# Kernel tuning notes

Hardware: AMD Instinct MI355X
Metric: run time of the kernel (lower is better)

## Reference

```python
import jax, jax.numpy as jnp
import numpy as np

B, N, F, L = 8, 2048, 128, 2
SLOPE = 0.1  # LeakyReLU negative slope

def lrelu(v):
    return jnp.where(v >= 0, v, SLOPE * v)

def setup_inputs() -> dict:
    key = jax.random.key(0)
    ks = jax.random.split(key, 7)
    scale = 1.0 / np.sqrt(F)
    return {
        "x": jax.random.normal(ks[0], (B, N, F), dtype=jnp.float32),
        "W3": jax.random.normal(ks[1], (L, F, F), dtype=jnp.float32) * scale,
        "b3": jnp.zeros((L, F), dtype=jnp.float32),
        "W4": jax.random.normal(ks[2], (L, F, F), dtype=jnp.float32) * scale,
        "b4": jnp.zeros((L, F), dtype=jnp.float32),
        "W5": jax.random.normal(ks[3], (L, F, F), dtype=jnp.float32) * scale,
        "b5": jnp.zeros((L, F), dtype=jnp.float32),
    }

def reference(x, W3, b3, W4, b4, W5, b5):
    # GraphStack of L GraphLayer modules, mes_type '0':
    #   weight_ij = dot(LeakyReLU(g3(n_i)), LeakyReLU(g4(n_j)))
    #   message_i = mean_{j != i} weight_ij * n_j
    #   n_i_out   = LeakyReLU(g5(message_i)) + n_i
    n = x.shape[1]
    for l in range(W3.shape[0]):
        w1 = lrelu(jnp.einsum('bnf,fg->bng', x, W3[l]) + b3[l])  # [B,N,F]
        w2 = lrelu(jnp.einsum('bnf,fg->bng', x, W4[l]) + b4[l])  # [B,N,F]
        wt = jnp.einsum('bif,bjf->bij', w1, w2)                  # pairwise weights [B,N,N]
        diag = jnp.einsum('bif,bif->bi', w1, w2)                 # self weights to exclude
        msg = (jnp.einsum('bij,bjf->bif', wt, x) - diag[..., None] * x) / (n - 1)
        x = lrelu(jnp.einsum('bif,fg->big', msg, W5[l]) + b5[l]) + x
    return x
```

## Files before the change

### kernel.cpp

```cpp
#include <hip/hip_runtime.h>

#define BB 8
#define NN 2048
#define FF 128
#define NL 2
#define SLOPE 0.1f
#define NROW (BB * NN)
#define XS_STRIDE 136

typedef __attribute__((ext_vector_type(8))) short short8;
typedef __attribute__((ext_vector_type(4))) float f32x4;

__device__ __forceinline__ float lrelu(float v) { return v >= 0.f ? v : SLOPE * v; }

__device__ __forceinline__ ushort f2bf(float f) {
    uint u = __float_as_uint(f);
    return (ushort)((u + 0x7fffu + ((u >> 16) & 1u)) >> 16);
}

__global__ __launch_bounds__(256) void k_prep(
    const float* __restrict__ W3, const float* __restrict__ W4,
    const float* __restrict__ W5, ushort* __restrict__ Wt)
{
    const int idx = blockIdx.x * 256 + threadIdx.x;
    const int m = idx >> 14;
    const int rem = idx & 16383;
    const int f = rem & 127;
    const int g = rem >> 7;
    const int l = m / 3, w = m % 3;
    const float* src = (w == 0) ? W3 : (w == 1) ? W4 : W5;
    Wt[m * 16384 + g * 128 + f] = f2bf(src[l * 16384 + f * 128 + g]);
}

__global__ __launch_bounds__(512) void k_w12(
    const float* __restrict__ x, const ushort* __restrict__ w3t,
    const ushort* __restrict__ w4t, const float* __restrict__ b3,
    const float* __restrict__ b4, ushort* __restrict__ w1b,
    ushort* __restrict__ w2t, ushort* __restrict__ xt,
    float* __restrict__ diag)
{
    __shared__ ushort xs[64 * XS_STRIDE];
    __shared__ float diag_s[64];

    const int tid = threadIdx.x;
    const int row0 = blockIdx.x * 64;
    const int b = row0 >> 11;
    const int jloc0 = row0 & 2047;

    if (tid < 64) diag_s[tid] = 0.f;

    const float4* xg4 = (const float4*)(x + (size_t)row0 * FF);
#pragma unroll
    for (int i = 0; i < 4; i++) {
        const int f4 = i * 512 + tid;
        const int row = f4 >> 5;
        const int k = (f4 & 31) * 4;
        float4 v = xg4[f4];
        ushort4 h;
        h.x = f2bf(v.x); h.y = f2bf(v.y); h.z = f2bf(v.z); h.w = f2bf(v.w);
        *(ushort4*)&xs[row * XS_STRIDE + k] = h;
    }
    __syncthreads();

    {
        const int g = tid >> 2;
        const int h = tid & 3;
        uint p[8];
#pragma unroll
        for (int jj = 0; jj < 8; jj++) {
            const uint lo = xs[(h * 16 + jj * 2) * XS_STRIDE + g];
            const uint hi = xs[(h * 16 + jj * 2 + 1) * XS_STRIDE + g];
            p[jj] = lo | (hi << 16);
        }
        uint4* dst = (uint4*)&xt[(size_t)b * (FF * NN) + (size_t)g * NN + jloc0 + h * 16];
        dst[0] = make_uint4(p[0], p[1], p[2], p[3]);
        dst[1] = make_uint4(p[4], p[5], p[6], p[7]);
    }

    const int lane = tid & 63;
    const int wave = tid >> 6;
    const int c = lane & 15;
    const int quad = lane >> 4;
    const int n = wave * 16 + c;

    f32x4 acc1[4], acc2[4];
#pragma unroll
    for (int rt = 0; rt < 4; rt++) { acc1[rt] = (f32x4)0.f; acc2[rt] = (f32x4)0.f; }

#pragma unroll
    for (int kk = 0; kk < 4; kk++) {
        short8 bf3 = *(const short8*)&w3t[n * 128 + kk * 32 + quad * 8];
        short8 bf4 = *(const short8*)&w4t[n * 128 + kk * 32 + quad * 8];
#pragma unroll
        for (int rt = 0; rt < 4; rt++) {
            short8 a = *(const short8*)&xs[(rt * 16 + c) * XS_STRIDE + kk * 32 + quad * 8];
            acc1[rt] = __builtin_amdgcn_mfma_f32_16x16x32_bf16(a, bf3, acc1[rt], 0, 0, 0);
            acc2[rt] = __builtin_amdgcn_mfma_f32_16x16x32_bf16(a, bf4, acc2[rt], 0, 0, 0);
        }
    }

    const int gcol = wave * 16 + c;
    const float bb3 = b3[gcol], bb4 = b4[gcol];
    float dpar[4][4];

#pragma unroll
    for (int rt = 0; rt < 4; rt++) {
        ushort w2p[4];
#pragma unroll
        for (int r = 0; r < 4; r++) {
            const float v1 = lrelu(acc1[rt][r] + bb3);
            const float v2 = lrelu(acc2[rt][r] + bb4);
            const int grow = row0 + rt * 16 + quad * 4 + r;
            w1b[(size_t)grow * FF + gcol] = f2bf(v1);
            w2p[r] = f2bf(v2);
            dpar[rt][r] = v1 * v2;
        }
        const uint lo = (uint)w2p[0] | ((uint)w2p[1] << 16);
        const uint hi = (uint)w2p[2] | ((uint)w2p[3] << 16);
        uint2* dst = (uint2*)&w2t[(size_t)b * (FF * NN) + (size_t)gcol * NN +
                                  jloc0 + rt * 16 + quad * 4];
        *dst = make_uint2(lo, hi);
    }

#pragma unroll
    for (int rt = 0; rt < 4; rt++) {
#pragma unroll
        for (int r = 0; r < 4; r++) {
            float dp = dpar[rt][r];
            dp += __shfl_xor(dp, 1, 64);
            dp += __shfl_xor(dp, 2, 64);
            dp += __shfl_xor(dp, 4, 64);
            dp += __shfl_xor(dp, 8, 64);
            if (c == 0) atomicAdd(&diag_s[rt * 16 + quad * 4 + r], dp);
        }
    }
    __syncthreads();
    if (tid < 64) diag[row0 + tid] = diag_s[tid];
}

__global__ __launch_bounds__(256) void k_S2(
    const ushort* __restrict__ xt, const ushort* __restrict__ w2t,
    ushort* __restrict__ St)
{
    __shared__ float red[4][512];
    const int tid = threadIdx.x;
    const int lane = tid & 63;
    const int wave = tid >> 6;
    const int c = lane & 15;
    const int quad = lane >> 4;

    const int b  = blockIdx.x >> 5;
    const int gq = (blockIdx.x >> 3) & 3;
    const int fs = blockIdx.x & 7;

    const ushort* xtb = xt + (size_t)b * (FF * NN);
    const ushort* w2b = w2t + (size_t)b * (FF * NN);

    const int j0 = wave * 512 + quad * 8;
    const ushort* a0p = &xtb[(gq * 32 + c) * NN + j0];
    const ushort* a1p = &xtb[(gq * 32 + 16 + c) * NN + j0];
    const ushort* bp  = &w2b[(fs * 16 + c) * NN + j0];

    f32x4 acc0 = (f32x4)0.f, acc1 = (f32x4)0.f;
#pragma unroll
    for (int it = 0; it < 16; it++) {
        short8 a0 = *(const short8*)(a0p + it * 32);
        short8 a1 = *(const short8*)(a1p + it * 32);
        short8 bf = *(const short8*)(bp + it * 32);
        acc0 = __builtin_amdgcn_mfma_f32_16x16x32_bf16(a0, bf, acc0, 0, 0, 0);
        acc1 = __builtin_amdgcn_mfma_f32_16x16x32_bf16(a1, bf, acc1, 0, 0, 0);
    }

#pragma unroll
    for (int r = 0; r < 4; r++) {
        red[wave][(quad * 4 + r) * 16 + c] = acc0[r];
        red[wave][(16 + quad * 4 + r) * 16 + c] = acc1[r];
    }
    __syncthreads();

#pragma unroll
    for (int i = 0; i < 2; i++) {
        const int idx = i * 256 + tid;
        const float s = red[0][idx] + red[1][idx] + red[2][idx] + red[3][idx];
        const int gl = idx >> 4;
        const int fl = idx & 15;
        St[(size_t)b * (FF * FF) + (size_t)(gq * 32 + gl) * FF + fs * 16 + fl] = f2bf(s);
    }
}

__global__ __launch_bounds__(512) void k_out(
    const float* __restrict__ x, const ushort* __restrict__ w1b,
    const ushort* __restrict__ St, const float* __restrict__ diag,
    const ushort* __restrict__ w5t, const float* __restrict__ b5,
    float* __restrict__ out)
{
    __shared__ ushort w1s[64 * XS_STRIDE];
    __shared__ ushort ms[64 * XS_STRIDE];

    const int tid = threadIdx.x;
    const int row0 = blockIdx.x * 64;
    const int b = row0 >> 11;
    const ushort* Sb = St + (size_t)b * (FF * FF);

#pragma unroll
    for (int i = 0; i < 2; i++) {
        const int off = (i * 512 + tid) * 8;
        const int row = off >> 7;
        const int k = off & 127;
        short8 v = *(const short8*)&w1b[(size_t)row0 * FF + off];
        *(short8*)&w1s[row * XS_STRIDE + k] = v;
    }
    __syncthreads();

    const int lane = tid & 63;
    const int wave = tid >> 6;
    const int c = lane & 15;
    const int quad = lane >> 4;
    const int n = wave * 16 + c;

    f32x4 accm[4];
#pragma unroll
    for (int rt = 0; rt < 4; rt++) accm[rt] = (f32x4)0.f;

#pragma unroll
    for (int kk = 0; kk < 4; kk++) {
        short8 bf = *(const short8*)&Sb[n * 128 + kk * 32 + quad * 8];
#pragma unroll
        for (int rt = 0; rt < 4; rt++) {
            short8 a = *(const short8*)&w1s[(rt * 16 + c) * XS_STRIDE + kk * 32 + quad * 8];
            accm[rt] = __builtin_amdgcn_mfma_f32_16x16x32_bf16(a, bf, accm[rt], 0, 0, 0);
        }
    }

    const float inv = 1.f / (float)(NN - 1);
    const int gcol = wave * 16 + c;
    float xsv[4][4];
#pragma unroll
    for (int rt = 0; rt < 4; rt++) {
        float dg[4];
#pragma unroll
        for (int r = 0; r < 4; r++) dg[r] = diag[row0 + rt * 16 + quad * 4 + r];
#pragma unroll
        for (int r = 0; r < 4; r++) {
            const int lrow = rt * 16 + quad * 4 + r;
            const float xv = x[(size_t)(row0 + lrow) * FF + gcol];
            xsv[rt][r] = xv;
            const float m = (accm[rt][r] - dg[r] * xv) * inv;
            ms[lrow * XS_STRIDE + gcol] = f2bf(m);
        }
    }
    __syncthreads();

    f32x4 acc2[4];
#pragma unroll
    for (int rt = 0; rt < 4; rt++) acc2[rt] = (f32x4)0.f;

#pragma unroll
    for (int kk = 0; kk < 4; kk++) {
        short8 bf = *(const short8*)&w5t[n * 128 + kk * 32 + quad * 8];
#pragma unroll
        for (int rt = 0; rt < 4; rt++) {
            short8 a = *(const short8*)&ms[(rt * 16 + c) * XS_STRIDE + kk * 32 + quad * 8];
            acc2[rt] = __builtin_amdgcn_mfma_f32_16x16x32_bf16(a, bf, acc2[rt], 0, 0, 0);
        }
    }

    const float bb = b5[gcol];
#pragma unroll
    for (int rt = 0; rt < 4; rt++) {
#pragma unroll
        for (int r = 0; r < 4; r++) {
            const int grow = row0 + rt * 16 + quad * 4 + r;
            out[(size_t)grow * FF + gcol] = lrelu(acc2[rt][r] + bb) + xsv[rt][r];
        }
    }
}

__global__ __launch_bounds__(512) void k_out_w12(
    const float* __restrict__ x, const ushort* __restrict__ w1b_in,
    const ushort* __restrict__ St, const float* __restrict__ diag_in,
    const ushort* __restrict__ w5t, const float* __restrict__ b5,
    float* __restrict__ out,
    const ushort* __restrict__ w3t, const ushort* __restrict__ w4t,
    const float* __restrict__ b3, const float* __restrict__ b4,
    ushort* __restrict__ w1b, ushort* __restrict__ w2t,
    ushort* __restrict__ xt, float* __restrict__ diag)
{
    __shared__ ushort sA[64 * XS_STRIDE];
    __shared__ ushort sB[64 * XS_STRIDE];
    __shared__ float diag_s[64];

    const int tid = threadIdx.x;
    const int row0 = blockIdx.x * 64;
    const int b = row0 >> 11;
    const int jloc0 = row0 & 2047;
    const ushort* Sb = St + (size_t)b * (FF * FF);

    if (tid < 64) diag_s[tid] = 0.f;

#pragma unroll
    for (int i = 0; i < 2; i++) {
        const int off = (i * 512 + tid) * 8;
        const int row = off >> 7;
        const int k = off & 127;
        short8 v = *(const short8*)&w1b_in[(size_t)row0 * FF + off];
        *(short8*)&sA[row * XS_STRIDE + k] = v;
    }
    __syncthreads();

    const int lane = tid & 63;
    const int wave = tid >> 6;
    const int c = lane & 15;
    const int quad = lane >> 4;
    const int n = wave * 16 + c;
    const int gcol = wave * 16 + c;

    f32x4 accm[4];
#pragma unroll
    for (int rt = 0; rt < 4; rt++) accm[rt] = (f32x4)0.f;

#pragma unroll
    for (int kk = 0; kk < 4; kk++) {
        short8 bf = *(const short8*)&Sb[n * 128 + kk * 32 + quad * 8];
#pragma unroll
        for (int rt = 0; rt < 4; rt++) {
            short8 a = *(const short8*)&sA[(rt * 16 + c) * XS_STRIDE + kk * 32 + quad * 8];
            accm[rt] = __builtin_amdgcn_mfma_f32_16x16x32_bf16(a, bf, accm[rt], 0, 0, 0);
        }
    }

    const float inv = 1.f / (float)(NN - 1);
    float xsv[4][4];
#pragma unroll
    for (int rt = 0; rt < 4; rt++) {
        float dg[4];
#pragma unroll
        for (int r = 0; r < 4; r++) dg[r] = diag_in[row0 + rt * 16 + quad * 4 + r];
#pragma unroll
        for (int r = 0; r < 4; r++) {
            const int lrow = rt * 16 + quad * 4 + r;
            const float xv = x[(size_t)(row0 + lrow) * FF + gcol];
            xsv[rt][r] = xv;
            const float m = (accm[rt][r] - dg[r] * xv) * inv;
            sB[lrow * XS_STRIDE + gcol] = f2bf(m);
        }
    }
    __syncthreads();

    f32x4 acc2[4];
#pragma unroll
    for (int rt = 0; rt < 4; rt++) acc2[rt] = (f32x4)0.f;

#pragma unroll
    for (int kk = 0; kk < 4; kk++) {
        short8 bf = *(const short8*)&w5t[n * 128 + kk * 32 + quad * 8];
#pragma unroll
        for (int rt = 0; rt < 4; rt++) {
            short8 a = *(const short8*)&sB[(rt * 16 + c) * XS_STRIDE + kk * 32 + quad * 8];
            acc2[rt] = __builtin_amdgcn_mfma_f32_16x16x32_bf16(a, bf, acc2[rt], 0, 0, 0);
        }
    }

    const float bb = b5[gcol];
#pragma unroll
    for (int rt = 0; rt < 4; rt++) {
#pragma unroll
        for (int r = 0; r < 4; r++) {
            const int lrow = rt * 16 + quad * 4 + r;
            const float ov = lrelu(acc2[rt][r] + bb) + xsv[rt][r];
            out[(size_t)(row0 + lrow) * FF + gcol] = ov;
            sA[lrow * XS_STRIDE + gcol] = f2bf(ov);
        }
    }
    __syncthreads();

    {
        const int g = tid >> 2;
        const int h = tid & 3;
        uint p[8];
#pragma unroll
        for (int jj = 0; jj < 8; jj++) {
            const uint lo = sA[(h * 16 + jj * 2) * XS_STRIDE + g];
            const uint hi = sA[(h * 16 + jj * 2 + 1) * XS_STRIDE + g];
            p[jj] = lo | (hi << 16);
        }
        uint4* dst = (uint4*)&xt[(size_t)b * (FF * NN) + (size_t)g * NN + jloc0 + h * 16];
        dst[0] = make_uint4(p[0], p[1], p[2], p[3]);
        dst[1] = make_uint4(p[4], p[5], p[6], p[7]);
    }

    f32x4 acc1n[4], acc2n[4];
#pragma unroll
    for (int rt = 0; rt < 4; rt++) { acc1n[rt] = (f32x4)0.f; acc2n[rt] = (f32x4)0.f; }

#pragma unroll
    for (int kk = 0; kk < 4; kk++) {
        short8 bf3 = *(const short8*)&w3t[n * 128 + kk * 32 + quad * 8];
        short8 bf4 = *(const short8*)&w4t[n * 128 + kk * 32 + quad * 8];
#pragma unroll
        for (int rt = 0; rt < 4; rt++) {
            short8 a = *(const short8*)&sA[(rt * 16 + c) * XS_STRIDE + kk * 32 + quad * 8];
            acc1n[rt] = __builtin_amdgcn_mfma_f32_16x16x32_bf16(a, bf3, acc1n[rt], 0, 0, 0);
            acc2n[rt] = __builtin_amdgcn_mfma_f32_16x16x32_bf16(a, bf4, acc2n[rt], 0, 0, 0);
        }
    }

    const float bb3 = b3[gcol], bb4 = b4[gcol];
    float dpar[4][4];
#pragma unroll
    for (int rt = 0; rt < 4; rt++) {
        ushort w2p[4];
#pragma unroll
        for (int r = 0; r < 4; r++) {
            const float v1 = lrelu(acc1n[rt][r] + bb3);
            const float v2 = lrelu(acc2n[rt][r] + bb4);
            const int grow = row0 + rt * 16 + quad * 4 + r;
            w1b[(size_t)grow * FF + gcol] = f2bf(v1);
            w2p[r] = f2bf(v2);
            dpar[rt][r] = v1 * v2;
        }
        const uint lo = (uint)w2p[0] | ((uint)w2p[1] << 16);
        const uint hi = (uint)w2p[2] | ((uint)w2p[3] << 16);
        uint2* dst = (uint2*)&w2t[(size_t)b * (FF * NN) + (size_t)gcol * NN +
                                  jloc0 + rt * 16 + quad * 4];
        *dst = make_uint2(lo, hi);
    }

#pragma unroll
    for (int rt = 0; rt < 4; rt++) {
#pragma unroll
        for (int r = 0; r < 4; r++) {
            float dp = dpar[rt][r];
            dp += __shfl_xor(dp, 1, 64);
            dp += __shfl_xor(dp, 2, 64);
            dp += __shfl_xor(dp, 4, 64);
            dp += __shfl_xor(dp, 8, 64);
            if (c == 0) atomicAdd(&diag_s[rt * 16 + quad * 4 + r], dp);
        }
    }
    __syncthreads();
    if (tid < 64) diag[row0 + tid] = diag_s[tid];
}

extern "C" void kernel_launch(void* const* d_in, const int* in_sizes, int n_in,
                              void* d_out, int out_size, void* d_ws, size_t ws_size,
                              hipStream_t stream)
{
    const float* x  = (const float*)d_in[0];
    const float* W3 = (const float*)d_in[1];
    const float* b3 = (const float*)d_in[2];
    const float* W4 = (const float*)d_in[3];
    const float* b4 = (const float*)d_in[4];
    const float* W5 = (const float*)d_in[5];
    const float* b5 = (const float*)d_in[6];
    float* out = (float*)d_out;

    char* ws = (char*)d_ws;
    ushort* w1b   = (ushort*)(ws);
    ushort* w2t   = (ushort*)(ws + ((size_t)4  << 20));
    ushort* xt    = (ushort*)(ws + ((size_t)8  << 20));
    float*  diag  = (float*) (ws + ((size_t)12 << 20));
    ushort* St    = (ushort*)(ws + ((size_t)13 << 20));
    ushort* Wt    = (ushort*)(ws + ((size_t)14 << 20));

    const ushort* w3t0 = Wt;
    const ushort* w4t0 = Wt + 16384;
    const ushort* w5t0 = Wt + 2 * 16384;
    const ushort* w3t1 = Wt + 3 * 16384;
    const ushort* w4t1 = Wt + 4 * 16384;
    const ushort* w5t1 = Wt + 5 * 16384;

    const int rowBlocks = NROW / 64;

    k_prep<<<384, 256, 0, stream>>>(W3, W4, W5, Wt);

    k_w12<<<rowBlocks, 512, 0, stream>>>(x, w3t0, w4t0, b3, b4, w1b, w2t, xt, diag);
    k_S2<<<256, 256, 0, stream>>>(xt, w2t, St);
    k_out_w12<<<rowBlocks, 512, 0, stream>>>(x, w1b, St, diag, w5t0, b5, out,
                                             w3t1, w4t1, b3 + FF, b4 + FF,
                                             w1b, w2t, xt, diag);
    k_S2<<<256, 256, 0, stream>>>(xt, w2t, St);
    k_out<<<rowBlocks, 512, 0, stream>>>(out, w1b, St, diag, w5t1, b5 + FF, out);
}
```

Measured before the change: 120.6 us.

## Fuse all stages into one cooperative persistent kernel with grid syncs

```diff
diff --git a/kernel.cpp b/kernel.cpp
--- a/kernel.cpp
+++ b/kernel.cpp
@@ -1,9 +1,11 @@
 #include <hip/hip_runtime.h>
+#include <hip/hip_cooperative_groups.h>
+
+namespace cg = cooperative_groups;
 
 #define BB 8
 #define NN 2048
 #define FF 128
-#define NL 2
 #define SLOPE 0.1f
 #define NROW (BB * NN)
 #define XS_STRIDE 136
@@ -18,428 +20,408 @@
     return (ushort)((u + 0x7fffu + ((u >> 16) & 1u)) >> 16);
 }
 
-__global__ __launch_bounds__(256) void k_prep(
-    const float* __restrict__ W3, const float* __restrict__ W4,
-    const float* __restrict__ W5, ushort* __restrict__ Wt)
+__device__ __forceinline__ void s2_phase(
+    const ushort* __restrict__ xt, const ushort* __restrict__ w2t,
+    ushort* __restrict__ St, float* red,
+    int bid, int tid, int wave, int c, int quad)
 {
-    const int idx = blockIdx.x * 256 + threadIdx.x;
-    const int m = idx >> 14;
-    const int rem = idx & 16383;
-    const int f = rem & 127;
-    const int g = rem >> 7;
-    const int l = m / 3, w = m % 3;
-    const float* src = (w == 0) ? W3 : (w == 1) ? W4 : W5;
-    Wt[m * 16384 + g * 128 + f] = f2bf(src[l * 16384 + f * 128 + g]);
+    const int b  = bid >> 5;
+    const int gq = (bid >> 3) & 3;
+    const int fs = bid & 7;
+
+    const ushort* xtb = xt + (size_t)b * (FF * NN);
+    const ushort* w2b = w2t + (size_t)b * (FF * NN);
+
+    const int j0 = wave * 256 + quad * 8;
+    const ushort* a0p = &xtb[(gq * 32 + c) * NN + j0];
+    const ushort* a1p = &xtb[(gq * 32 + 16 + c) * NN + j0];
+    const ushort* bp  = &w2b[(fs * 16 + c) * NN + j0];
+
+    f32x4 acc0 = (f32x4)0.f, acc1 = (f32x4)0.f;
+#pragma unroll
+    for (int it = 0; it < 8; it++) {
+        short8 a0 = *(const short8*)(a0p + it * 32);
+        short8 a1 = *(const short8*)(a1p + it * 32);
+        short8 bf = *(const short8*)(bp + it * 32);
+        acc0 = __builtin_amdgcn_mfma_f32_16x16x32_bf16(a0, bf, acc0, 0, 0, 0);
+        acc1 = __builtin_amdgcn_mfma_f32_16x16x32_bf16(a1, bf, acc1, 0, 0, 0);
+    }
+
+#pragma unroll
+    for (int r = 0; r < 4; r++) {
+        red[wave * 512 + (quad * 4 + r) * 16 + c] = acc0[r];
+        red[wave * 512 + (16 + quad * 4 + r) * 16 + c] = acc1[r];
+    }
+    __syncthreads();
+
+    {
+        float s = 0.f;
+#pragma unroll
+        for (int w = 0; w < 8; w++) s += red[w * 512 + tid];
+        const int gl = tid >> 4;
+        const int fl = tid & 15;
+        St[(size_t)b * (FF * FF) + (size_t)(gq * 32 + gl) * FF + fs * 16 + fl] = f2bf(s);
+    }
+    __syncthreads();
 }
 
-__global__ __launch_bounds__(512) void k_w12(
-    const float* __restrict__ x, const ushort* __restrict__ w3t,
-    const ushort* __restrict__ w4t, const float* __restrict__ b3,
-    const float* __restrict__ b4, ushort* __restrict__ w1b,
-    ushort* __restrict__ w2t, ushort* __restrict__ xt,
-    float* __restrict__ diag)
+__global__ __launch_bounds__(512) void k_all(
+    const float* __restrict__ x,
+    const float* __restrict__ W3, const float* __restrict__ b3,
+    const float* __restrict__ W4, const float* __restrict__ b4,
+    const float* __restrict__ W5, const float* __restrict__ b5,
+    float* __restrict__ out,
+    ushort* __restrict__ w1b, ushort* __restrict__ w2t,
+    ushort* __restrict__ xt, float* __restrict__ diag,
+    ushort* __restrict__ St, ushort* __restrict__ Wt)
 {
-    __shared__ ushort xs[64 * XS_STRIDE];
+    __shared__ ushort smem[2 * 64 * XS_STRIDE];
     __shared__ float diag_s[64];
 
+    cg::grid_group grid = cg::this_grid();
+
     const int tid = threadIdx.x;
-    const int row0 = blockIdx.x * 64;
-    const int b = row0 >> 11;
-    const int jloc0 = row0 & 2047;
-
-    if (tid < 64) diag_s[tid] = 0.f;
-
-    const float4* xg4 = (const float4*)(x + (size_t)row0 * FF);
-#pragma unroll
-    for (int i = 0; i < 4; i++) {
-        const int f4 = i * 512 + tid;
-        const int row = f4 >> 5;
-        const int k = (f4 & 31) * 4;
-        float4 v = xg4[f4];
-        ushort4 h;
-        h.x = f2bf(v.x); h.y = f2bf(v.y); h.z = f2bf(v.z); h.w = f2bf(v.w);
-        *(ushort4*)&xs[row * XS_STRIDE + k] = h;
-    }
-    __syncthreads();
-
-    {
-        const int g = tid >> 2;
-        const int h = tid & 3;
-        uint p[8];
-#pragma unroll
-        for (int jj = 0; jj < 8; jj++) {
-            const uint lo = xs[(h * 16 + jj * 2) * XS_STRIDE + g];
-            const uint hi = xs[(h * 16 + jj * 2 + 1) * XS_STRIDE + g];
-            p[jj] = lo | (hi << 16);
-        }
-        uint4* dst = (uint4*)&xt[(size_t)b * (FF * NN) + (size_t)g * NN + jloc0 + h * 16];
-        dst[0] = make_uint4(p[0], p[1], p[2], p[3]);
-        dst[1] = make_uint4(p[4], p[5], p[6], p[7]);
-    }
-
+    const int bid = blockIdx.x;
     const int lane = tid & 63;
     const int wave = tid >> 6;
     const int c = lane & 15;
     const int quad = lane >> 4;
     const int n = wave * 16 + c;
-
-    f32x4 acc1[4], acc2[4];
-#pragma unroll
-    for (int rt = 0; rt < 4; rt++) { acc1[rt] = (f32x4)0.f; acc2[rt] = (f32x4)0.f; }
-
-#pragma unroll
-    for (int kk = 0; kk < 4; kk++) {
-        short8 bf3 = *(const short8*)&w3t[n * 128 + kk * 32 + quad * 8];
-        short8 bf4 = *(const short8*)&w4t[n * 128 + kk * 32 + quad * 8];
-#pragma unroll
-        for (int rt = 0; rt < 4; rt++) {
-            short8 a = *(const short8*)&xs[(rt * 16 + c) * XS_STRIDE + kk * 32 + quad * 8];
-            acc1[rt] = __builtin_amdgcn_mfma_f32_16x16x32_bf16(a, bf3, acc1[rt], 0, 0, 0);
-            acc2[rt] = __builtin_amdgcn_mfma_f32_16x16x32_bf16(a, bf4, acc2[rt], 0, 0, 0);
-        }
-    }
-
-    const int gcol = wave * 16 + c;
-    const float bb3 = b3[gcol], bb4 = b4[gcol];
-    float dpar[4][4];
-
-#pragma unroll
-    for (int rt = 0; rt < 4; rt++) {
-        ushort w2p[4];
-#pragma unroll
-        for (int r = 0; r < 4; r++) {
-            const float v1 = lrelu(acc1[rt][r] + bb3);
-            const float v2 = lrelu(acc2[rt][r] + bb4);
-            const int grow = row0 + rt * 16 + quad * 4 + r;
-            w1b[(size_t)grow * FF + gcol] = f2bf(v1);
-            w2p[r] = f2bf(v2);
-            dpar[rt][r] = v1 * v2;
-        }
-        const uint lo = (uint)w2p[0] | ((uint)w2p[1] << 16);
-        const uint hi = (uint)w2p[2] | ((uint)w2p[3] << 16);
-        uint2* dst = (uint2*)&w2t[(size_t)b * (FF * NN) + (size_t)gcol * NN +
-                                  jloc0 + rt * 16 + quad * 4];
-        *dst = make_uint2(lo, hi);
-    }
-
-#pragma unroll
-    for (int rt = 0; rt < 4; rt++) {
-#pragma unroll
-        for (int r = 0; r < 4; r++) {
-            float dp = dpar[rt][r];
-            dp += __shfl_xor(dp, 1, 64);
-            dp += __shfl_xor(dp, 2, 64);
-            dp += __shfl_xor(dp, 4, 64);
-            dp += __shfl_xor(dp, 8, 64);
-            if (c == 0) atomicAdd(&diag_s[rt * 16 + quad * 4 + r], dp);
-        }
-    }
-    __syncthreads();
-    if (tid < 64) diag[row0 + tid] = diag_s[tid];
-}
-
-__global__ __launch_bounds__(256) void k_S2(
-    const ushort* __restrict__ xt, const ushort* __restrict__ w2t,
-    ushort* __restrict__ St)
-{
-    __shared__ float red[4][512];
-    const int tid = threadIdx.x;
-    const int lane = tid & 63;
-    const int wave = tid >> 6;
-    const int c = lane & 15;
-    const int quad = lane >> 4;
-
-    const int b  = blockIdx.x >> 5;
-    const int gq = (blockIdx.x >> 3) & 3;
-    const int fs = blockIdx.x & 7;
-
-    const ushort* xtb = xt + (size_t)b * (FF * NN);
-    const ushort* w2b = w2t + (size_t)b * (FF * NN);
-
-    const int j0 = wave * 512 + quad * 8;
-    const ushort* a0p = &xtb[(gq * 32 + c) * NN + j0];
-    const ushort* a1p = &xtb[(gq * 32 + 16 + c) * NN + j0];
-    const ushort* bp  = &w2b[(fs * 16 + c) * NN + j0];
-
-    f32x4 acc0 = (f32x4)0.f, acc1 = (f32x4)0.f;
-#pragma unroll
-    for (int it = 0; it < 16; it++) {
-        short8 a0 = *(const short8*)(a0p + it * 32);
-        short8 a1 = *(const short8*)(a1p + it * 32);
-        short8 bf = *(const short8*)(bp + it * 32);
-        acc0 = __builtin_amdgcn_mfma_f32_16x16x32_bf16(a0, bf, acc0, 0, 0, 0);
-        acc1 = __builtin_amdgcn_mfma_f32_16x16x32_bf16(a1, bf, acc1, 0, 0, 0);
-    }
-
-#pragma unroll
-    for (int r = 0; r < 4; r++) {
-        red[wave][(quad * 4 + r) * 16 + c] = acc0[r];
-        red[wave][(16 + quad * 4 + r) * 16 + c] = acc1[r];
-    }
-    __syncthreads();
-
-#pragma unroll
-    for (int i = 0; i < 2; i++) {
-        const int idx = i * 256 + tid;
-        const float s = red[0][idx] + red[1][idx] + red[2][idx] + red[3][idx];
-        const int gl = idx >> 4;
-        const int fl = idx & 15;
-        St[(size_t)b * (FF * FF) + (size_t)(gq * 32 + gl) * FF + fs * 16 + fl] = f2bf(s);
-    }
-}
-
-__global__ __launch_bounds__(512) void k_out(
-    const float* __restrict__ x, const ushort* __restrict__ w1b,
-    const ushort* __restrict__ St, const float* __restrict__ diag,
-    const ushort* __restrict__ w5t, const float* __restrict__ b5,
-    float* __restrict__ out)
-{
-    __shared__ ushort w1s[64 * XS_STRIDE];
-    __shared__ ushort ms[64 * XS_STRIDE];
-
-    const int tid = threadIdx.x;
-    const int row0 = blockIdx.x * 64;
-    const int b = row0 >> 11;
-    const ushort* Sb = St + (size_t)b * (FF * FF);
-
-#pragma unroll
-    for (int i = 0; i < 2; i++) {
-        const int off = (i * 512 + tid) * 8;
-        const int row = off >> 7;
-        const int k = off & 127;
-        short8 v = *(const short8*)&w1b[(size_t)row0 * FF + off];
-        *(short8*)&w1s[row * XS_STRIDE + k] = v;
-    }
-    __syncthreads();
-
-    const int lane = tid & 63;
-    const int wave = tid >> 6;
-    const int c = lane & 15;
-    const int quad = lane >> 4;
-    const int n = wave * 16 + c;
-
-    f32x4 accm[4];
-#pragma unroll
-    for (int rt = 0; rt < 4; rt++) accm[rt] = (f32x4)0.f;
-
-#pragma unroll
-    for (int kk = 0; kk < 4; kk++) {
-        short8 bf = *(const short8*)&Sb[n * 128 + kk * 32 + quad * 8];
-#pragma unroll
-        for (int rt = 0; rt < 4; rt++) {
-            short8 a = *(const short8*)&w1s[(rt * 16 + c) * XS_STRIDE + kk * 32 + quad * 8];
-            accm[rt] = __builtin_amdgcn_mfma_f32_16x16x32_bf16(a, bf, accm[rt], 0, 0, 0);
-        }
-    }
-
-    const float inv = 1.f / (float)(NN - 1);
-    const int gcol = wave * 16 + c;
-    float xsv[4][4];
-#pragma unroll
-    for (int rt = 0; rt < 4; rt++) {
-        float dg[4];
-#pragma unroll
-        for (int r = 0; r < 4; r++) dg[r] = diag[row0 + rt * 16 + quad * 4 + r];
-#pragma unroll
-        for (int r = 0; r < 4; r++) {
-            const int lrow = rt * 16 + quad * 4 + r;
-            const float xv = x[(size_t)(row0 + lrow) * FF + gcol];
-            xsv[rt][r] = xv;
-            const float m = (accm[rt][r] - dg[r] * xv) * inv;
-            ms[lrow * XS_STRIDE + gcol] = f2bf(m);
-        }
-    }
-    __syncthreads();
-
-    f32x4 acc2[4];
-#pragma unroll
-    for (int rt = 0; rt < 4; rt++) acc2[rt] = (f32x4)0.f;
-
-#pragma unroll
-    for (int kk = 0; kk < 4; kk++) {
-        short8 bf = *(const short8*)&w5t[n * 128 + kk * 32 + quad * 8];
-#pragma unroll
-        for (int rt = 0; rt < 4; rt++) {
-            short8 a = *(const short8*)&ms[(rt * 16 + c) * XS_STRIDE + kk * 32 + quad * 8];
-            acc2[rt] = __builtin_amdgcn_mfma_f32_16x16x32_bf16(a, bf, acc2[rt], 0, 0, 0);
-        }
-    }
-
-    const float bb = b5[gcol];
-#pragma unroll
-    for (int rt = 0; rt < 4; rt++) {
-#pragma unroll
-        for (int r = 0; r < 4; r++) {
-            const int grow = row0 + rt * 16 + quad * 4 + r;
-            out[(size_t)grow * FF + gcol] = lrelu(acc2[rt][r] + bb) + xsv[rt][r];
-        }
-    }
-}
-
-__global__ __launch_bounds__(512) void k_out_w12(
-    const float* __restrict__ x, const ushort* __restrict__ w1b_in,
-    const ushort* __restrict__ St, const float* __restrict__ diag_in,
-    const ushort* __restrict__ w5t, const float* __restrict__ b5,
-    float* __restrict__ out,
-    const ushort* __restrict__ w3t, const ushort* __restrict__ w4t,
-    const float* __restrict__ b3, const float* __restrict__ b4,
-    ushort* __restrict__ w1b, ushort* __restrict__ w2t,
-    ushort* __restrict__ xt, float* __restrict__ diag)
-{
-    __shared__ ushort sA[64 * XS_STRIDE];
-    __shared__ ushort sB[64 * XS_STRIDE];
-    __shared__ float diag_s[64];
-
-    const int tid = threadIdx.x;
-    const int row0 = blockIdx.x * 64;
+    const int gcol = n;
+
+    const ushort* w3t0 = Wt;
+    const ushort* w4t0 = Wt + 16384;
+    const ushort* w5t0 = Wt + 2 * 16384;
+    const ushort* w3t1 = Wt + 3 * 16384;
+    const ushort* w4t1 = Wt + 4 * 16384;
+    const ushort* w5t1 = Wt + 5 * 16384;
+
+    const int row0 = bid * 64;
     const int b = row0 >> 11;
     const int jloc0 = row0 & 2047;
-    const ushort* Sb = St + (size_t)b * (FF * FF);
-
-    if (tid < 64) diag_s[tid] = 0.f;
-
-#pragma unroll
-    for (int i = 0; i < 2; i++) {
-        const int off = (i * 512 + tid) * 8;
-        const int row = off >> 7;
-        const int k = off & 127;
-        short8 v = *(const short8*)&w1b_in[(size_t)row0 * FF + off];
-        *(short8*)&sA[row * XS_STRIDE + k] = v;
-    }
-    __syncthreads();
-
-    const int lane = tid & 63;
-    const int wave = tid >> 6;
-    const int c = lane & 15;
-    const int quad = lane >> 4;
-    const int n = wave * 16 + c;
-    const int gcol = wave * 16 + c;
-
-    f32x4 accm[4];
-#pragma unroll
-    for (int rt = 0; rt < 4; rt++) accm[rt] = (f32x4)0.f;
-
-#pragma unroll
-    for (int kk = 0; kk < 4; kk++) {
-        short8 bf = *(const short8*)&Sb[n * 128 + kk * 32 + quad * 8];
-#pragma unroll
-        for (int rt = 0; rt < 4; rt++) {
-            short8 a = *(const short8*)&sA[(rt * 16 + c) * XS_STRIDE + kk * 32 + quad * 8];
-            accm[rt] = __builtin_amdgcn_mfma_f32_16x16x32_bf16(a, bf, accm[rt], 0, 0, 0);
-        }
-    }
-
     const float inv = 1.f / (float)(NN - 1);
-    float xsv[4][4];
-#pragma unroll
-    for (int rt = 0; rt < 4; rt++) {
-        float dg[4];
-#pragma unroll
-        for (int r = 0; r < 4; r++) dg[r] = diag_in[row0 + rt * 16 + quad * 4 + r];
-#pragma unroll
-        for (int r = 0; r < 4; r++) {
-            const int lrow = rt * 16 + quad * 4 + r;
-            const float xv = x[(size_t)(row0 + lrow) * FF + gcol];
-            xsv[rt][r] = xv;
-            const float m = (accm[rt][r] - dg[r] * xv) * inv;
-            sB[lrow * XS_STRIDE + gcol] = f2bf(m);
-        }
-    }
-    __syncthreads();
-
-    f32x4 acc2[4];
-#pragma unroll
-    for (int rt = 0; rt < 4; rt++) acc2[rt] = (f32x4)0.f;
-
-#pragma unroll
-    for (int kk = 0; kk < 4; kk++) {
-        short8 bf = *(const short8*)&w5t[n * 128 + kk * 32 + quad * 8];
-#pragma unroll
-        for (int rt = 0; rt < 4; rt++) {
-            short8 a = *(const short8*)&sB[(rt * 16 + c) * XS_STRIDE + kk * 32 + quad * 8];
-            acc2[rt] = __builtin_amdgcn_mfma_f32_16x16x32_bf16(a, bf, acc2[rt], 0, 0, 0);
-        }
-    }
-
-    const float bb = b5[gcol];
-#pragma unroll
-    for (int rt = 0; rt < 4; rt++) {
-#pragma unroll
-        for (int r = 0; r < 4; r++) {
-            const int lrow = rt * 16 + quad * 4 + r;
-            const float ov = lrelu(acc2[rt][r] + bb) + xsv[rt][r];
-            out[(size_t)(row0 + lrow) * FF + gcol] = ov;
-            sA[lrow * XS_STRIDE + gcol] = f2bf(ov);
-        }
-    }
-    __syncthreads();
 
     {
-        const int g = tid >> 2;
-        const int h = tid & 3;
-        uint p[8];
-#pragma unroll
-        for (int jj = 0; jj < 8; jj++) {
-            const uint lo = sA[(h * 16 + jj * 2) * XS_STRIDE + g];
-            const uint hi = sA[(h * 16 + jj * 2 + 1) * XS_STRIDE + g];
-            p[jj] = lo | (hi << 16);
-        }
-        uint4* dst = (uint4*)&xt[(size_t)b * (FF * NN) + (size_t)g * NN + jloc0 + h * 16];
-        dst[0] = make_uint4(p[0], p[1], p[2], p[3]);
-        dst[1] = make_uint4(p[4], p[5], p[6], p[7]);
-    }
-
-    f32x4 acc1n[4], acc2n[4];
-#pragma unroll
-    for (int rt = 0; rt < 4; rt++) { acc1n[rt] = (f32x4)0.f; acc2n[rt] = (f32x4)0.f; }
-
-#pragma unroll
-    for (int kk = 0; kk < 4; kk++) {
-        short8 bf3 = *(const short8*)&w3t[n * 128 + kk * 32 + quad * 8];
-        short8 bf4 = *(const short8*)&w4t[n * 128 + kk * 32 + quad * 8];
-#pragma unroll
-        for (int rt = 0; rt < 4; rt++) {
-            short8 a = *(const short8*)&sA[(rt * 16 + c) * XS_STRIDE + kk * 32 + quad * 8];
-            acc1n[rt] = __builtin_amdgcn_mfma_f32_16x16x32_bf16(a, bf3, acc1n[rt], 0, 0, 0);
-            acc2n[rt] = __builtin_amdgcn_mfma_f32_16x16x32_bf16(a, bf4, acc2n[rt], 0, 0, 0);
-        }
-    }
-
-    const float bb3 = b3[gcol], bb4 = b4[gcol];
-    float dpar[4][4];
-#pragma unroll
-    for (int rt = 0; rt < 4; rt++) {
-        ushort w2p[4];
-#pragma unroll
-        for (int r = 0; r < 4; r++) {
-            const float v1 = lrelu(acc1n[rt][r] + bb3);
-            const float v2 = lrelu(acc2n[rt][r] + bb4);
-            const int grow = row0 + rt * 16 + quad * 4 + r;
-            w1b[(size_t)grow * FF + gcol] = f2bf(v1);
-            w2p[r] = f2bf(v2);
-            dpar[rt][r] = v1 * v2;
-        }
-        const uint lo = (uint)w2p[0] | ((uint)w2p[1] << 16);
-        const uint hi = (uint)w2p[2] | ((uint)w2p[3] << 16);
-        uint2* dst = (uint2*)&w2t[(size_t)b * (FF * NN) + (size_t)gcol * NN +
-                                  jloc0 + rt * 16 + quad * 4];
-        *dst = make_uint2(lo, hi);
-    }
-
-#pragma unroll
-    for (int rt = 0; rt < 4; rt++) {
-#pragma unroll
-        for (int r = 0; r < 4; r++) {
-            float dp = dpar[rt][r];
-            dp += __shfl_xor(dp, 1, 64);
-            dp += __shfl_xor(dp, 2, 64);
-            dp += __shfl_xor(dp, 4, 64);
-            dp += __shfl_xor(dp, 8, 64);
-            if (c == 0) atomicAdd(&diag_s[rt * 16 + quad * 4 + r], dp);
-        }
-    }
-    __syncthreads();
-    if (tid < 64) diag[row0 + tid] = diag_s[tid];
+        const int idx = bid * 512 + tid;
+        if (idx < 98304) {
+            const int m = idx >> 14;
+            const int rem = idx & 16383;
+            const int f = rem & 127;
+            const int g = rem >> 7;
+            const int l = m / 3, w = m % 3;
+            const float* src = (w == 0) ? W3 : (w == 1) ? W4 : W5;
+            Wt[m * 16384 + g * 128 + f] = f2bf(src[l * 16384 + f * 128 + g]);
+        }
+    }
+    grid.sync();
+
+    {
+        ushort* xs = smem;
+        if (tid < 64) diag_s[tid] = 0.f;
+
+        const float4* xg4 = (const float4*)(x + (size_t)row0 * FF);
+#pragma unroll
+        for (int i = 0; i < 4; i++) {
+            const int f4 = i * 512 + tid;
+            const int row = f4 >> 5;
+            const int k = (f4 & 31) * 4;
+            float4 v = xg4[f4];
+            ushort4 h;
+            h.x = f2bf(v.x); h.y = f2bf(v.y); h.z = f2bf(v.z); h.w = f2bf(v.w);
+            *(ushort4*)&xs[row * XS_STRIDE + k] = h;
+        }
+        __syncthreads();
+
+        {
+            const int g = tid >> 2;
+            const int h = tid & 3;
+            uint p[8];
+#pragma unroll
+            for (int jj = 0; jj < 8; jj++) {
+                const uint lo = xs[(h * 16 + jj * 2) * XS_STRIDE + g];
+                const uint hi = xs[(h * 16 + jj * 2 + 1) * XS_STRIDE + g];
+                p[jj] = lo | (hi << 16);
+            }
+            uint4* dst = (uint4*)&xt[(size_t)b * (FF * NN) + (size_t)g * NN + jloc0 + h * 16];
+            dst[0] = make_uint4(p[0], p[1], p[2], p[3]);
+            dst[1] = make_uint4(p[4], p[5], p[6], p[7]);
+        }
+
+        f32x4 acc1[4], acc2[4];
+#pragma unroll
+        for (int rt = 0; rt < 4; rt++) { acc1[rt] = (f32x4)0.f; acc2[rt] = (f32x4)0.f; }
+
+#pragma unroll
+        for (int kk = 0; kk < 4; kk++) {
+            short8 bf3 = *(const short8*)&w3t0[n * 128 + kk * 32 + quad * 8];
+            short8 bf4 = *(const short8*)&w4t0[n * 128 + kk * 32 + quad * 8];
+#pragma unroll
+            for (int rt = 0; rt < 4; rt++) {
+                short8 a = *(const short8*)&xs[(rt * 16 + c) * XS_STRIDE + kk * 32 + quad * 8];
+                acc1[rt] = __builtin_amdgcn_mfma_f32_16x16x32_bf16(a, bf3, acc1[rt], 0, 0, 0);
+                acc2[rt] = __builtin_amdgcn_mfma_f32_16x16x32_bf16(a, bf4, acc2[rt], 0, 0, 0);
+            }
+        }
+
+        const float bb3 = b3[gcol], bb4 = b4[gcol];
+        float dpar[4][4];
+#pragma unroll
+        for (int rt = 0; rt < 4; rt++) {
+            ushort w2p[4];
+#pragma unroll
+            for (int r = 0; r < 4; r++) {
+                const float v1 = lrelu(acc1[rt][r] + bb3);
+                const float v2 = lrelu(acc2[rt][r] + bb4);
+                const int grow = row0 + rt * 16 + quad * 4 + r;
+                w1b[(size_t)grow * FF + gcol] = f2bf(v1);
+                w2p[r] = f2bf(v2);
+                dpar[rt][r] = v1 * v2;
+            }
+            const uint lo = (uint)w2p[0] | ((uint)w2p[1] << 16);
+            const uint hi = (uint)w2p[2] | ((uint)w2p[3] << 16);
+            uint2* dst = (uint2*)&w2t[(size_t)b * (FF * NN) + (size_t)gcol * NN +
+                                      jloc0 + rt * 16 + quad * 4];
+            *dst = make_uint2(lo, hi);
+        }
+
+#pragma unroll
+        for (int rt = 0; rt < 4; rt++) {
+#pragma unroll
+            for (int r = 0; r < 4; r++) {
+                float dp = dpar[rt][r];
+                dp += __shfl_xor(dp, 1, 64);
+                dp += __shfl_xor(dp, 2, 64);
+                dp += __shfl_xor(dp, 4, 64);
+                dp += __shfl_xor(dp, 8, 64);
+                if (c == 0) atomicAdd(&diag_s[rt * 16 + quad * 4 + r], dp);
+            }
+        }
+        __syncthreads();
+        if (tid < 64) diag[row0 + tid] = diag_s[tid];
+    }
+    grid.sync();
+
+    s2_phase(xt, w2t, St, (float*)smem, bid, tid, wave, c, quad);
+    grid.sync();
+
+    {
+        ushort* sA = smem;
+        ushort* sB = smem + 64 * XS_STRIDE;
+        const ushort* Sb = St + (size_t)b * (FF * FF);
+
+        if (tid < 64) diag_s[tid] = 0.f;
+
+#pragma unroll
+        for (int i = 0; i < 2; i++) {
+            const int off = (i * 512 + tid) * 8;
+            const int row = off >> 7;
+            const int k = off & 127;
+            short8 v = *(const short8*)&w1b[(size_t)row0 * FF + off];
+            *(short8*)&sA[row * XS_STRIDE + k] = v;
+        }
+        __syncthreads();
+
+        f32x4 accm[4];
+#pragma unroll
+        for (int rt = 0; rt < 4; rt++) accm[rt] = (f32x4)0.f;
+
+#pragma unroll
+        for (int kk = 0; kk < 4; kk++) {
+            short8 bf = *(const short8*)&Sb[n * 128 + kk * 32 + quad * 8];
+#pragma unroll
+            for (int rt = 0; rt < 4; rt++) {
+                short8 a = *(const short8*)&sA[(rt * 16 + c) * XS_STRIDE + kk * 32 + quad * 8];
+                accm[rt] = __builtin_amdgcn_mfma_f32_16x16x32_bf16(a, bf, accm[rt], 0, 0, 0);
+            }
+        }
+
+        float xsv[4][4];
+#pragma unroll
+        for (int rt = 0; rt < 4; rt++) {
+            float dg[4];
+#pragma unroll
+            for (int r = 0; r < 4; r++) dg[r] = diag[row0 + rt * 16 + quad * 4 + r];
+#pragma unroll
+            for (int r = 0; r < 4; r++) {
+                const int lrow = rt * 16 + quad * 4 + r;
+                const float xv = x[(size_t)(row0 + lrow) * FF + gcol];
+                xsv[rt][r] = xv;
+                const float m = (accm[rt][r] - dg[r] * xv) * inv;
+                sB[lrow * XS_STRIDE + gcol] = f2bf(m);
+            }
+        }
+        __syncthreads();
+
+        f32x4 acc2[4];
+#pragma unroll
+        for (int rt = 0; rt < 4; rt++) acc2[rt] = (f32x4)0.f;
+
+#pragma unroll
+        for (int kk = 0; kk < 4; kk++) {
+            short8 bf = *(const short8*)&w5t0[n * 128 + kk * 32 + quad * 8];
+#pragma unroll
+            for (int rt = 0; rt < 4; rt++) {
+                short8 a = *(const short8*)&sB[(rt * 16 + c) * XS_STRIDE + kk * 32 + quad * 8];
+                acc2[rt] = __builtin_amdgcn_mfma_f32_16x16x32_bf16(a, bf, acc2[rt], 0, 0, 0);
+            }
+        }
+
+        const float bb = b5[gcol];
+#pragma unroll
+        for (int rt = 0; rt < 4; rt++) {
+#pragma unroll
+            for (int r = 0; r < 4; r++) {
+                const int lrow = rt * 16 + quad * 4 + r;
+                const float ov = lrelu(acc2[rt][r] + bb) + xsv[rt][r];
+                out[(size_t)(row0 + lrow) * FF + gcol] = ov;
+                sA[lrow * XS_STRIDE + gcol] = f2bf(ov);
+            }
+        }
+        __syncthreads();
+
+        {
+            const int g = tid >> 2;
+            const int h = tid & 3;
+            uint p[8];
+#pragma unroll
+            for (int jj = 0; jj < 8; jj++) {
+                const uint lo = sA[(h * 16 + jj * 2) * XS_STRIDE + g];
+                const uint hi = sA[(h * 16 + jj * 2 + 1) * XS_STRIDE + g];
+                p[jj] = lo | (hi << 16);
+            }
+            uint4* dst = (uint4*)&xt[(size_t)b * (FF * NN) + (size_t)g * NN + jloc0 + h * 16];
+            dst[0] = make_uint4(p[0], p[1], p[2], p[3]);
+            dst[1] = make_uint4(p[4], p[5], p[6], p[7]);
+        }
+
+        f32x4 acc1n[4], acc2n[4];
+#pragma unroll
+        for (int rt = 0; rt < 4; rt++) { acc1n[rt] = (f32x4)0.f; acc2n[rt] = (f32x4)0.f; }
+
+#pragma unroll
+        for (int kk = 0; kk < 4; kk++) {
+            short8 bf3 = *(const short8*)&w3t1[n * 128 + kk * 32 + quad * 8];
+            short8 bf4 = *(const short8*)&w4t1[n * 128 + kk * 32 + quad * 8];
+#pragma unroll
+            for (int rt = 0; rt < 4; rt++) {
+                short8 a = *(const short8*)&sA[(rt * 16 + c) * XS_STRIDE + kk * 32 + quad * 8];
+                acc1n[rt] = __builtin_amdgcn_mfma_f32_16x16x32_bf16(a, bf3, acc1n[rt], 0, 0, 0);
+                acc2n[rt] = __builtin_amdgcn_mfma_f32_16x16x32_bf16(a, bf4, acc2n[rt], 0, 0, 0);
+            }
+        }
+
+        const float bb3 = b3[FF + gcol], bb4 = b4[FF + gcol];
+        float dpar[4][4];
+#pragma unroll
+        for (int rt = 0; rt < 4; rt++) {
+            ushort w2p[4];
+#pragma unroll
+            for (int r = 0; r < 4; r++) {
+                const float v1 = lrelu(acc1n[rt][r] + bb3);
+                const float v2 = lrelu(acc2n[rt][r] + bb4);
+                const int grow = row0 + rt * 16 + quad * 4 + r;
+                w1b[(size_t)grow * FF + gcol] = f2bf(v1);
+                w2p[r] = f2bf(v2);
+                dpar[rt][r] = v1 * v2;
+            }
+            const uint lo = (uint)w2p[0] | ((uint)w2p[1] << 16);
+            const uint hi = (uint)w2p[2] | ((uint)w2p[3] << 16);
+            uint2* dst = (uint2*)&w2t[(size_t)b * (FF * NN) + (size_t)gcol * NN +
+                                      jloc0 + rt * 16 + quad * 4];
+            *dst = make_uint2(lo, hi);
+        }
+
+#pragma unroll
+        for (int rt = 0; rt < 4; rt++) {
+#pragma unroll
+            for (int r = 0; r < 4; r++) {
+                float dp = dpar[rt][r];
+                dp += __shfl_xor(dp, 1, 64);
+                dp += __shfl_xor(dp, 2, 64);
+                dp += __shfl_xor(dp, 4, 64);
+                dp += __shfl_xor(dp, 8, 64);
+                if (c == 0) atomicAdd(&diag_s[rt * 16 + quad * 4 + r], dp);
+            }
+        }
+        __syncthreads();
+        if (tid < 64) diag[row0 + tid] = diag_s[tid];
+        __syncthreads();
+    }
+    grid.sync();
+
+    s2_phase(xt, w2t, St, (float*)smem, bid, tid, wave, c, quad);
+    grid.sync();
+
+    {
+        ushort* w1s = smem;
+        ushort* ms = smem + 64 * XS_STRIDE;
+        const ushort* Sb = St + (size_t)b * (FF * FF);
+
+#pragma unroll
+        for (int i = 0; i < 2; i++) {
+            const int off = (i * 512 + tid) * 8;
+            const int row = off >> 7;
+            const int k = off & 127;
+            short8 v = *(const short8*)&w1b[(size_t)row0 * FF + off];
+            *(short8*)&w1s[row * XS_STRIDE + k] = v;
+        }
+        __syncthreads();
+
+        f32x4 accm[4];
+#pragma unroll
+        for (int rt = 0; rt < 4; rt++) accm[rt] = (f32x4)0.f;
+
+#pragma unroll
+        for (int kk = 0; kk < 4; kk++) {
+            short8 bf = *(const short8*)&Sb[n * 128 + kk * 32 + quad * 8];
+#pragma unroll
+            for (int rt = 0; rt < 4; rt++) {
+                short8 a = *(const short8*)&w1s[(rt * 16 + c) * XS_STRIDE + kk * 32 + quad * 8];
+                accm[rt] = __builtin_amdgcn_mfma_f32_16x16x32_bf16(a, bf, accm[rt], 0, 0, 0);
+            }
+        }
+
+        float xsv[4][4];
+#pragma unroll
+        for (int rt = 0; rt < 4; rt++) {
+            float dg[4];
+#pragma unroll
+            for (int r = 0; r < 4; r++) dg[r] = diag[row0 + rt * 16 + quad * 4 + r];
+#pragma unroll
+            for (int r = 0; r < 4; r++) {
+                const int lrow = rt * 16 + quad * 4 + r;
+                const float xv = out[(size_t)(row0 + lrow) * FF + gcol];
+                xsv[rt][r] = xv;
+                const float m = (accm[rt][r] - dg[r] * xv) * inv;
+                ms[lrow * XS_STRIDE + gcol] = f2bf(m);
+            }
+        }
+        __syncthreads();
+
+        f32x4 acc2[4];
+#pragma unroll
+        for (int rt = 0; rt < 4; rt++) acc2[rt] = (f32x4)0.f;
+
+#pragma unroll
+        for (int kk = 0; kk < 4; kk++) {
+            short8 bf = *(const short8*)&w5t1[n * 128 + kk * 32 + quad * 8];
+#pragma unroll
+            for (int rt = 0; rt < 4; rt++) {
+                short8 a = *(const short8*)&ms[(rt * 16 + c) * XS_STRIDE + kk * 32 + quad * 8];
+                acc2[rt] = __builtin_amdgcn_mfma_f32_16x16x32_bf16(a, bf, acc2[rt], 0, 0, 0);
+            }
+        }
+
+        const float bb = b5[FF + gcol];
+#pragma unroll
+        for (int rt = 0; rt < 4; rt++) {
+#pragma unroll
+            for (int r = 0; r < 4; r++) {
+                const int grow = row0 + rt * 16 + quad * 4 + r;
+                out[(size_t)grow * FF + gcol] = lrelu(acc2[rt][r] + bb) + xsv[rt][r];
+            }
+        }
+    }
 }
 
 extern "C" void kernel_launch(void* const* d_in, const int* in_sizes, int n_in,
@@ -463,22 +445,11 @@
     ushort* St    = (ushort*)(ws + ((size_t)13 << 20));
     ushort* Wt    = (ushort*)(ws + ((size_t)14 << 20));
 
-    const ushort* w3t0 = Wt;
-    const ushort* w4t0 = Wt + 16384;
-    const ushort* w5t0 = Wt + 2 * 16384;
-    const ushort* w3t1 = Wt + 3 * 16384;
-    const ushort* w4t1 = Wt + 4 * 16384;
-    const ushort* w5t1 = Wt + 5 * 16384;
-
-    const int rowBlocks = NROW / 64;
-
-    k_prep<<<384, 256, 0, stream>>>(W3, W4, W5, Wt);
-
-    k_w12<<<rowBlocks, 512, 0, stream>>>(x, w3t0, w4t0, b3, b4, w1b, w2t, xt, diag);
-    k_S2<<<256, 256, 0, stream>>>(xt, w2t, St);
-    k_out_w12<<<rowBlocks, 512, 0, stream>>>(x, w1b, St, diag, w5t0, b5, out,
-                                             w3t1, w4t1, b3 + FF, b4 + FF,
-                                             w1b, w2t, xt, diag);
-    k_S2<<<256, 256, 0, stream>>>(xt, w2t, St);
-    k_out<<<rowBlocks, 512, 0, stream>>>(out, w1b, St, diag, w5t1, b5 + FF, out);
+    void* args[] = {
+        (void*)&x, (void*)&W3, (void*)&b3, (void*)&W4, (void*)&b4,
+        (void*)&W5, (void*)&b5, (void*)&out,
+        (void*)&w1b, (void*)&w2t, (void*)&xt, (void*)&diag,
+        (void*)&St, (void*)&Wt
+    };
+    hipLaunchCooperativeKernel((void*)k_all, dim3(256), dim3(512), args, 0, stream);
 }
```

After: 263.9 us. 2.19x slower.
